# Performance work log

Measured on AMD Instinct MI355X. Metric: run time of the kernel, lower is better.

The kernel has to match this reference:

```python
import jax, jax.numpy as jnp
import numpy as np
import math

# ---- architecture constants (match init_kwargs defaults of OfficialMamba3SISO) ----
D_MODEL = 1024
D_STATE = 128
EXPAND = 2
HEADDIM = 64
NGROUPS = 1
D_INNER = EXPAND * D_MODEL              # 2048
NHEADS = D_INNER // HEADDIM             # 32
ROPE_FRACTION = 0.5
SPLIT = int(D_STATE * ROPE_FRACTION)    # rotary span of the state dim
SPLIT -= SPLIT % 2                      # 64
NUM_ANGLES = SPLIT // 2                 # 32
A_FLOOR = 1e-4
EPS = 1e-5
DT_MIN, DT_MAX, DT_INIT_FLOOR = 1e-3, 1e-1, 1e-4
D_IN_PROJ = 2 * D_INNER + 2 * D_STATE * NGROUPS + 3 * NHEADS + NUM_ANGLES  # 4480


def _rmsnorm(x, w):
    xf = x.astype(jnp.float32)
    return xf * jax.lax.rsqrt(jnp.mean(xf * xf, axis=-1, keepdims=True) + EPS) * w


def _rope(v, theta):
    # rotate first SPLIT dims of the state axis by cumulative angles theta [..., NUM_ANGLES]
    v1 = v[..., :NUM_ANGLES]
    v2 = v[..., NUM_ANGLES:SPLIT]
    rest = v[..., SPLIT:]
    c, s = jnp.cos(theta), jnp.sin(theta)
    return jnp.concatenate([v1 * c - v2 * s, v1 * s + v2 * c, rest], axis=-1)


def setup_inputs() -> dict:
    key = jax.random.key(0)
    ks = jax.random.split(key, 6)
    b, l = 2, 1024
    u = jax.random.normal(ks[0], (b, l, D_MODEL), jnp.float32)
    W_in = jax.random.normal(ks[1], (D_IN_PROJ, D_MODEL), jnp.float32) * 0.02
    W_out = jax.random.normal(ks[2], (D_MODEL, D_INNER), jnp.float32) * 0.02
    # dt_bias init exactly as in the torch module
    _dt = jnp.exp(jax.random.uniform(ks[3], (NHEADS,), jnp.float32)
                  * (math.log(DT_MAX) - math.log(DT_MIN)) + math.log(DT_MIN))
    _dt = jnp.clip(_dt, DT_INIT_FLOOR, None)
    dt_bias = _dt + jnp.log(-jnp.expm1(-_dt))
    B_bias = jnp.ones((NHEADS, D_STATE), jnp.float32)   # mimo_rank=1 squeezed
    C_bias = jnp.ones((NHEADS, D_STATE), jnp.float32)
    B_norm_w = jnp.ones((D_STATE,), jnp.float32)
    C_norm_w = jnp.ones((D_STATE,), jnp.float32)
    D_param = jnp.ones((NHEADS,), jnp.float32)
    return {"u": u, "W_in": W_in, "W_out": W_out, "dt_bias": dt_bias,
            "B_bias": B_bias, "C_bias": C_bias, "B_norm_w": B_norm_w,
            "C_norm_w": C_norm_w, "D_param": D_param}


def reference(u, W_in, W_out, dt_bias, B_bias, C_bias, B_norm_w, C_norm_w, D_param):
    b, l, _ = u.shape
    proj = u @ W_in.T                                   # [b,l,4480]
    sizes = [D_INNER, D_INNER, D_STATE * NGROUPS, D_STATE * NGROUPS,
             NHEADS, NHEADS, NHEADS, NUM_ANGLES]
    splits = np.cumsum(sizes)[:-1]
    z, x, B, C, dd_dt, dd_A, trap, angles = jnp.split(proj, splits, axis=-1)
    z = z.reshape(b, l, NHEADS, HEADDIM)
    x = x.reshape(b, l, NHEADS, HEADDIM)
    B = B.reshape(b, l, NGROUPS, D_STATE)
    C = C.reshape(b, l, NGROUPS, D_STATE)

    a = -jax.nn.softplus(dd_A.astype(jnp.float32))
    a = jnp.minimum(a, -A_FLOOR)                        # [b,l,h]
    dt = jax.nn.softplus(dd_dt.astype(jnp.float32) + dt_bias)  # [b,l,h]
    adt = a * dt

    # RoPE-style angle cumsum: theta_t = sum_{s<=t} angle_s * dt_s (per head)
    theta = jnp.cumsum(angles[:, :, None, :].astype(jnp.float32) * dt[..., None], axis=1)  # [b,l,h,na]

    Bn = _rmsnorm(B, B_norm_w)                          # [b,l,g,n]
    Cn = _rmsnorm(C, C_norm_w)
    head_group = np.repeat(np.arange(NGROUPS), NHEADS // NGROUPS)
    Bh = Bn[:, :, head_group, :] + B_bias               # [b,l,h,n]
    Ch = Cn[:, :, head_group, :] + C_bias
    Bh = _rope(Bh, theta)
    Ch = _rope(Ch, theta)

    lam = jax.nn.sigmoid(trap.astype(jnp.float32))      # trapezoidal mixing, [b,l,h]
    g = jnp.exp(adt)                                    # decay, [b,l,h]

    xs = (jnp.moveaxis(x.astype(jnp.float32), 1, 0), jnp.moveaxis(Bh, 1, 0),
          jnp.moveaxis(Ch, 1, 0), jnp.moveaxis(dt, 1, 0),
          jnp.moveaxis(g, 1, 0), jnp.moveaxis(lam, 1, 0))
    h0 = jnp.zeros((b, NHEADS, HEADDIM, D_STATE), jnp.float32)
    bx0 = jnp.zeros_like(h0)

    def step(carry, inp):
        h, bx_prev = carry
        x_t, B_t, C_t, dt_t, g_t, lam_t = inp
        bx_t = x_t[..., :, None] * B_t[..., None, :]    # outer product [b,h,p,n]
        ge = g_t[..., None, None]
        dte = dt_t[..., None, None]
        le = lam_t[..., None, None]
        # generalized trapezoidal discretization (Mamba-3):
        # h_t = g_t h_{t-1} + dt_t * (lam_t B_t x_t + (1-lam_t) g_t B_{t-1} x_{t-1})
        h = ge * h + dte * (le * bx_t + (1.0 - le) * ge * bx_prev)
        y_t = jnp.einsum('bhpn,bhn->bhp', h, C_t)
        return (h, bx_t), y_t

    _, ys = jax.lax.scan(step, (h0, bx0), xs)
    y = jnp.moveaxis(ys, 0, 1) + D_param[:, None] * x   # skip term, [b,l,h,p]
    y = y * jax.nn.silu(z)                              # gated output (Z passed to kernel)
    y = y.reshape(b, l, D_INNER).astype(u.dtype)
    return y @ W_out.T
```

## Files before the change

kernel.cpp:

```cpp
#include <hip/hip_runtime.h>
#include <hip/hip_bf16.h>
#include <math.h>

#define BATCH 2
#define SEQ 1024
#define DMODEL 1024
#define DSTATE 128
#define HEADDIM 64
#define NHEADS 32
#define DINNER 2048
#define NUMANG 32
#define DPROJ 4480
#define CH 64
#define NCH 16
#define TAILSTART 4352
#define OFF_Z 0
#define OFF_X 2048
#define OFF_B 4096
#define OFF_C 4224
#define OFF_DT 4352
#define OFF_A 4384
#define OFF_TRAP 4416
#define OFF_ANG 4448

typedef __attribute__((ext_vector_type(8))) short bf16x8;
typedef __attribute__((ext_vector_type(4))) float f32x4;
typedef unsigned short u16;

__device__ __forceinline__ u16 f2bf(float f) {
  unsigned int u = __float_as_uint(f);
  u += 0x7FFFu + ((u >> 16) & 1u);
  return (u16)(u >> 16);
}
__device__ __forceinline__ float bf2f(u16 x) {
  return __uint_as_float(((unsigned int)x) << 16);
}

#define N4_U 524288
#define N4_WI 1146880
#define N4_WO 524288

__global__ __launch_bounds__(256) void cvt_all(const float* __restrict__ u,
                                               const float* __restrict__ Wi,
                                               const float* __restrict__ Wo,
                                               u16* __restrict__ ub16,
                                               u16* __restrict__ Wi16,
                                               u16* __restrict__ Wo16) {
  int i = blockIdx.x * 256 + threadIdx.x;
  const float4* src;
  ushort4* dst;
  int idx;
  if (i < N4_U) { src = (const float4*)u; dst = (ushort4*)ub16; idx = i; }
  else if (i < N4_U + N4_WI) { src = (const float4*)Wi; dst = (ushort4*)Wi16; idx = i - N4_U; }
  else if (i < N4_U + N4_WI + N4_WO) { src = (const float4*)Wo; dst = (ushort4*)Wo16; idx = i - N4_U - N4_WI; }
  else return;
  float4 v = src[idx];
  ushort4 o;
  o.x = f2bf(v.x); o.y = f2bf(v.y); o.z = f2bf(v.z); o.w = f2bf(v.w);
  dst[idx] = o;
}

__device__ __forceinline__ void gload_lds16(const void* g, void* l) {
  __builtin_amdgcn_global_load_lds(
      (const __attribute__((address_space(1))) unsigned int*)g,
      (__attribute__((address_space(3))) unsigned int*)l, 16, 0, 0);
}

__global__ __launch_bounds__(256) void gemm_proj64(const u16* __restrict__ A,
                                                   const u16* __restrict__ B,
                                                   u16* __restrict__ Cb,
                                                   float* __restrict__ tailF,
                                                   int M, int N, int K) {
  __shared__ u16 As[64 * 64];
  __shared__ u16 Bs[64 * 64];
  const int tid = threadIdx.x;
  const int lane = tid & 63, wave = tid >> 6;
  const int bm = blockIdx.y * 64, bn = blockIdx.x * 64;
  const int wm = (wave >> 1) * 32, wn = (wave & 1) * 32;
  const int srow = wave * 8 + (lane >> 3);
  const int scol = (((lane & 7) ^ ((lane >> 3) & 7)) * 8);
  const u16* Ab = A + (size_t)(bm + srow) * K + scol;
  const u16* Bb = B + (size_t)(bn + srow) * K + scol;
  u16* Asw = As + wave * 512;
  u16* Bsw = Bs + wave * 512;
  f32x4 acc[2][2];
#pragma unroll
  for (int i = 0; i < 2; ++i)
#pragma unroll
    for (int j = 0; j < 2; ++j) acc[i][j] = (f32x4){0.f, 0.f, 0.f, 0.f};
  const int fr = lane & 15, fq = lane >> 4, sw = fr & 7;

  for (int k0 = 0; k0 < K; k0 += 64) {
    __syncthreads();
#pragma unroll
    for (int it = 0; it < 2; ++it) {
      gload_lds16(Ab + (size_t)(it * 32) * K + k0, Asw + it * 2048);
      gload_lds16(Bb + (size_t)(it * 32) * K + k0, Bsw + it * 2048);
    }
    __syncthreads();
#pragma unroll
    for (int kh = 0; kh < 2; ++kh) {
      bf16x8 af[2], bfv[2];
#pragma unroll
      for (int i = 0; i < 2; ++i)
        af[i] = *(const bf16x8*)(As + (wm + i * 16 + fr) * 64 + (((kh * 4 + fq) ^ sw) * 8));
#pragma unroll
      for (int j = 0; j < 2; ++j)
        bfv[j] = *(const bf16x8*)(Bs + (wn + j * 16 + fr) * 64 + (((kh * 4 + fq) ^ sw) * 8));
#pragma unroll
      for (int i = 0; i < 2; ++i)
#pragma unroll
        for (int j = 0; j < 2; ++j)
          acc[i][j] = __builtin_amdgcn_mfma_f32_16x16x32_bf16(af[i], bfv[j], acc[i][j], 0, 0, 0);
    }
  }
  const int orow = bm + wm + fq * 4;
  const int ocol = bn + wn + fr;
  const bool tail = (bn >= TAILSTART);
#pragma unroll
  for (int i = 0; i < 2; ++i)
#pragma unroll
    for (int j = 0; j < 2; ++j)
#pragma unroll
      for (int r = 0; r < 4; ++r) {
        float v = acc[i][j][r];
        int row = orow + i * 16 + r, col = ocol + j * 16;
        Cb[(size_t)row * N + col] = f2bf(v);
        if (tail) tailF[(size_t)row * 128 + (col - TAILSTART)] = v;
      }
}

__global__ __launch_bounds__(256) void gemm_out64(const u16* __restrict__ A,
                                                  const u16* __restrict__ B,
                                                  float* __restrict__ C,
                                                  int M, int N, int K) {
  __shared__ u16 As[64 * 64];
  __shared__ u16 Bs[64 * 64];
  const int tid = threadIdx.x;
  const int lane = tid & 63, wave = tid >> 6;
  const int bm = blockIdx.y * 64, bn = blockIdx.x * 64;
  const int wm = (wave >> 1) * 32, wn = (wave & 1) * 32;
  const int srow = wave * 8 + (lane >> 3);
  const int scol = (((lane & 7) ^ ((lane >> 3) & 7)) * 8);
  const u16* Ab = A + (size_t)(bm + srow) * K + scol;
  const u16* Bb = B + (size_t)(bn + srow) * K + scol;
  u16* Asw = As + wave * 512;
  u16* Bsw = Bs + wave * 512;
  f32x4 acc[2][2];
#pragma unroll
  for (int i = 0; i < 2; ++i)
#pragma unroll
    for (int j = 0; j < 2; ++j) acc[i][j] = (f32x4){0.f, 0.f, 0.f, 0.f};
  const int fr = lane & 15, fq = lane >> 4, sw = fr & 7;

  for (int k0 = 0; k0 < K; k0 += 64) {
    __syncthreads();
#pragma unroll
    for (int it = 0; it < 2; ++it) {
      gload_lds16(Ab + (size_t)(it * 32) * K + k0, Asw + it * 2048);
      gload_lds16(Bb + (size_t)(it * 32) * K + k0, Bsw + it * 2048);
    }
    __syncthreads();
#pragma unroll
    for (int kh = 0; kh < 2; ++kh) {
      bf16x8 af[2], bfv[2];
#pragma unroll
      for (int i = 0; i < 2; ++i)
        af[i] = *(const bf16x8*)(As + (wm + i * 16 + fr) * 64 + (((kh * 4 + fq) ^ sw) * 8));
#pragma unroll
      for (int j = 0; j < 2; ++j)
        bfv[j] = *(const bf16x8*)(Bs + (wn + j * 16 + fr) * 64 + (((kh * 4 + fq) ^ sw) * 8));
#pragma unroll
      for (int i = 0; i < 2; ++i)
#pragma unroll
        for (int j = 0; j < 2; ++j)
          acc[i][j] = __builtin_amdgcn_mfma_f32_16x16x32_bf16(af[i], bfv[j], acc[i][j], 0, 0, 0);
    }
  }
  const int orow = bm + wm + fq * 4;
  const int ocol = bn + wn + fr;
#pragma unroll
  for (int i = 0; i < 2; ++i)
#pragma unroll
    for (int j = 0; j < 2; ++j)
#pragma unroll
      for (int r = 0; r < 4; ++r)
        C[(size_t)(orow + i * 16 + r) * N + ocol + j * 16] = acc[i][j][r];
}

__device__ __forceinline__ float softplusf(float x) {
  return fmaxf(x, 0.f) + log1pf(expf(-fabsf(x)));
}

__global__ __launch_bounds__(1024) void theta_kernel(const float* __restrict__ tailF,
                                                     const float* __restrict__ dt_bias,
                                                     float4* __restrict__ sc4,
                                                     float4* __restrict__ theta4) {
  __shared__ float4 part[16];
  __shared__ float4 part2[16];
  const int blk = blockIdx.x;
  const int bh = blk >> 3, kc = blk & 7;
  const int b = bh >> 5, h = bh & 31;
  const int l = threadIdx.x;
  const int lane = l & 63, w = l >> 6;
  const float* trow = tailF + (size_t)(b * SEQ + l) * 128;
  float ddt = trow[h];
  float dt = softplusf(ddt + dt_bias[h]);
  if (kc == 0) {
    float dda = trow[32 + h];
    float trp = trow[64 + h];
    float a = fminf(-softplusf(dda), -1e-4f);
    float adt = a * dt;
    float lam = 1.0f / (1.0f + expf(-trp));
    sc4[(size_t)bh * SEQ + l] = make_float4(dt, expf(adt), lam, adt);
  }
  float4 v = *(const float4*)(trow + 96 + kc * 4);
  v.x *= dt; v.y *= dt; v.z *= dt; v.w *= dt;
#pragma unroll
  for (int off = 1; off < 64; off <<= 1) {
    float tx = __shfl_up(v.x, off, 64);
    float ty = __shfl_up(v.y, off, 64);
    float tz = __shfl_up(v.z, off, 64);
    float tw = __shfl_up(v.w, off, 64);
    if (lane >= off) { v.x += tx; v.y += ty; v.z += tz; v.w += tw; }
  }
  if (lane == 63) part[w] = v;
  __syncthreads();
  if (l < 16) {
    float4 p = part[l];
#pragma unroll
    for (int off = 1; off < 16; off <<= 1) {
      float tx = __shfl_up(p.x, off, 16);
      float ty = __shfl_up(p.y, off, 16);
      float tz = __shfl_up(p.z, off, 16);
      float tw = __shfl_up(p.w, off, 16);
      if (l >= off) { p.x += tx; p.y += ty; p.z += tz; p.w += tw; }
    }
    part2[l] = p;
  }
  __syncthreads();
  if (w > 0) {
    float4 o = part2[w - 1];
    v.x += o.x; v.y += o.y; v.z += o.z; v.w += o.w;
  }
  theta4[((size_t)(b * SEQ + l) * NHEADS + h) * 8 + kc] = v;
}

__global__ __launch_bounds__(1024) void rope_kernel(const u16* __restrict__ proj16,
                                                    const float* __restrict__ theta,
                                                    const float* __restrict__ B_bias,
                                                    const float* __restrict__ C_bias,
                                                    const float* __restrict__ Bnw,
                                                    const float* __restrict__ Cnw,
                                                    u16* __restrict__ Bh,
                                                    u16* __restrict__ Ch) {
  const int bl = blockIdx.x;
  const int b = bl >> 10, l = bl & 1023;
  const int tid = threadIdx.x;
  __shared__ float sB[128], sC[128], red[4];
  __shared__ float cth[1024], sth[1024];
  float bv = 0.f, cv = 0.f;
  const size_t row = (size_t)bl * DPROJ;
  if (tid < 128) {
    bv = bf2f(proj16[row + OFF_B + tid]);
    cv = bf2f(proj16[row + OFF_C + tid]);
    float sb = bv * bv, sc = cv * cv;
    for (int m = 32; m; m >>= 1) { sb += __shfl_xor(sb, m); sc += __shfl_xor(sc, m); }
    const int wave = tid >> 6;
    if ((tid & 63) == 0) { red[wave * 2] = sb; red[wave * 2 + 1] = sc; }
  }
  {
    float th = theta[(size_t)bl * 1024 + tid];
    cth[tid] = cosf(th);
    sth[tid] = sinf(th);
  }
  __syncthreads();
  if (tid < 128) {
    float rb = rsqrtf((red[0] + red[2]) / 128.0f + 1e-5f);
    float rc = rsqrtf((red[1] + red[3]) / 128.0f + 1e-5f);
    sB[tid] = bv * rb * Bnw[tid];
    sC[tid] = cv * rc * Cnw[tid];
  }
  __syncthreads();
  const int h = tid >> 5;
  const int n0 = (tid & 31) * 4;
  float ob[4], oc[4];
  if (n0 < 32) {
#pragma unroll
    for (int j = 0; j < 4; ++j) {
      int n = n0 + j;
      float c = cth[h * 32 + n], s = sth[h * 32 + n];
      float b1 = sB[n] + B_bias[h * 128 + n];
      float b2 = sB[n + 32] + B_bias[h * 128 + n + 32];
      float c1 = sC[n] + C_bias[h * 128 + n];
      float c2 = sC[n + 32] + C_bias[h * 128 + n + 32];
      ob[j] = b1 * c - b2 * s;
      oc[j] = c1 * c - c2 * s;
    }
  } else if (n0 < 64) {
#pragma unroll
    for (int j = 0; j < 4; ++j) {
      int n = n0 + j, k = n - 32;
      float c = cth[h * 32 + k], s = sth[h * 32 + k];
      float b1 = sB[k] + B_bias[h * 128 + k];
      float b2 = sB[k + 32] + B_bias[h * 128 + k + 32];
      float c1 = sC[k] + C_bias[h * 128 + k];
      float c2 = sC[k + 32] + C_bias[h * 128 + k + 32];
      ob[j] = b1 * s + b2 * c;
      oc[j] = c1 * s + c2 * c;
    }
  } else {
#pragma unroll
    for (int j = 0; j < 4; ++j) {
      int n = n0 + j;
      ob[j] = sB[n] + B_bias[h * 128 + n];
      oc[j] = sC[n] + C_bias[h * 128 + n];
    }
  }
  size_t o = (((size_t)(b * NHEADS + h)) * SEQ + l) * DSTATE + n0;
  ushort4 vb = {f2bf(ob[0]), f2bf(ob[1]), f2bf(ob[2]), f2bf(ob[3])};
  ushort4 vc = {f2bf(oc[0]), f2bf(oc[1]), f2bf(oc[2]), f2bf(oc[3])};
  *(ushort4*)&Bh[o] = vb;
  *(ushort4*)&Ch[o] = vc;
}

#define SWB 136
#define SWS 72

__global__ __launch_bounds__(256) void chunk_kernel(
    const u16* __restrict__ proj16,
    const float4* __restrict__ sc4,
    const u16* __restrict__ Bh16,
    const u16* __restrict__ Ch16,
    u16* __restrict__ Ybuf,
    u16* __restrict__ dHT16,
    float* __restrict__ Gv_g,
    float2* __restrict__ de_g) {
  __shared__ u16 sCb[64 * SWB];
  __shared__ u16 sBb[64 * SWB];
  __shared__ u16 sBt[128 * SWS];
  __shared__ u16 sXt[64 * SWS];
  __shared__ u16 sSw[64 * SWS];
  __shared__ float sA[64], sW[64], sDL[64], sCV[64];

  const int blk = blockIdx.x;
  const int bh = blk >> 4, ch = blk & 15;
  const int b = bh >> 5, h = bh & 31;
  const int t0 = ch * CH;
  const int tid = threadIdx.x;
  const int lane = tid & 63, wave = tid >> 6;

  {
    const int row = tid >> 5;
    const int c4 = tid & 31;
#pragma unroll
    for (int pass = 0; pass < 8; ++pass) {
      int ll = pass * 8 + row;
      int l = t0 + ll;
      ushort4 cv = *(const ushort4*)&Ch16[((size_t)bh * SEQ + l) * DSTATE + c4 * 4];
      ushort4 bv = *(const ushort4*)&Bh16[((size_t)bh * SEQ + l) * DSTATE + c4 * 4];
      *(ushort4*)&sCb[ll * SWB + c4 * 4] = cv;
      *(ushort4*)&sBb[ll * SWB + c4 * 4] = bv;
      sBt[(c4 * 4 + 0) * SWS + ll] = bv.x;
      sBt[(c4 * 4 + 1) * SWS + ll] = bv.y;
      sBt[(c4 * 4 + 2) * SWS + ll] = bv.z;
      sBt[(c4 * 4 + 3) * SWS + ll] = bv.w;
    }
    const int xr = tid >> 2, xc = tid & 3;
    const u16* xrow = &proj16[(size_t)(b * SEQ + t0 + xr) * DPROJ + OFF_X + h * 64];
#pragma unroll
    for (int j = 0; j < 4; ++j) {
      ushort4 xv = *(const ushort4*)(xrow + xc * 16 + j * 4);
      int p = xc * 16 + j * 4;
      sXt[(p + 0) * SWS + xr] = xv.x;
      sXt[(p + 1) * SWS + xr] = xv.y;
      sXt[(p + 2) * SWS + xr] = xv.z;
      sXt[(p + 3) * SWS + xr] = xv.w;
    }
  }
  if (tid < 64) {
    float4 s = sc4[(size_t)bh * SEQ + t0 + tid];
    float dt = s.x, lam = s.z, adt = s.w;
    float A = adt;
#pragma unroll
    for (int off = 1; off < 64; off <<= 1) {
      float t = __shfl_up(A, off, 64);
      if (tid >= off) A += t;
    }
    float dtn = __shfl_down(dt, 1, 64);
    float lamn = __shfl_down(lam, 1, 64);
    float dl = dt * lam;
    float w = dl + dtn * (1.0f - lamn);
    if (tid == 63) w = 0.0f;
    float A63 = __shfl(A, 63, 64);
    float cv = (tid < 63) ? expf(A63 - A) * w : dl;
    sA[tid] = A; sW[tid] = w; sCV[tid] = cv; sDL[tid] = dl;
    Gv_g[((size_t)bh * NCH + ch) * 64 + tid] = expf(A);
    if (tid == 0) de_g[(size_t)bh * NCH + ch] = make_float2(expf(A63), dt * (1.0f - lam));
  }
  __syncthreads();

  const int fr = lane & 15, fq = lane >> 4;

  {
    f32x4 acc[4];
#pragma unroll
    for (int j = 0; j < 4; ++j) acc[j] = (f32x4){0.f, 0.f, 0.f, 0.f};
#pragma unroll
    for (int kc = 0; kc < 4; ++kc) {
      bf16x8 af = *(const bf16x8*)&sBb[(wave * 16 + fr) * SWB + kc * 32 + fq * 8];
#pragma unroll
      for (int j = 0; j < 4; ++j) {
        bf16x8 bf = *(const bf16x8*)&sCb[(j * 16 + fr) * SWB + kc * 32 + fq * 8];
        acc[j] = __builtin_amdgcn_mfma_f32_16x16x32_bf16(af, bf, acc[j], 0, 0, 0);
      }
    }
    const int sbase = wave * 16 + fq * 4;
#pragma unroll
    for (int j = 0; j < 4; ++j) {
      int t = j * 16 + fr;
      float At = sA[t], dlt = sDL[t];
#pragma unroll
      for (int r = 0; r < 4; ++r) {
        int ss = sbase + r;
        float f = (ss < t) ? expf(At - sA[ss]) * sW[ss] : ((ss == t) ? dlt : 0.0f);
        sSw[t * SWS + ss] = f2bf(acc[j][r] * f);
      }
    }
  }
  __syncthreads();

  {
    f32x4 acc[4];
#pragma unroll
    for (int j = 0; j < 4; ++j) acc[j] = (f32x4){0.f, 0.f, 0.f, 0.f};
#pragma unroll
    for (int kc = 0; kc < 2; ++kc) {
      bf16x8 af = *(const bf16x8*)&sSw[(wave * 16 + fr) * SWS + kc * 32 + fq * 8];
#pragma unroll
      for (int j = 0; j < 4; ++j) {
        bf16x8 bf = *(const bf16x8*)&sXt[(j * 16 + fr) * SWS + kc * 32 + fq * 8];
        acc[j] = __builtin_amdgcn_mfma_f32_16x16x32_bf16(af, bf, acc[j], 0, 0, 0);
      }
    }
    const int tr = t0 + wave * 16 + fq * 4;
#pragma unroll
    for (int j = 0; j < 4; ++j) {
      int p = j * 16 + fr;
#pragma unroll
      for (int r = 0; r < 4; ++r)
        Ybuf[(size_t)(b * SEQ + tr + r) * DINNER + h * 64 + p] = f2bf(acc[j][r]);
    }
  }
  __syncthreads();

  {
    const int p = tid >> 2;
    const int s0 = (tid & 3) * 16;
#pragma unroll
    for (int k = 0; k < 16; ++k) {
      int s = s0 + k;
      sXt[p * SWS + s] = f2bf(bf2f(sXt[p * SWS + s]) * sCV[s]);
    }
  }
  __syncthreads();

  {
    f32x4 acc[8];
#pragma unroll
    for (int j = 0; j < 8; ++j) acc[j] = (f32x4){0.f, 0.f, 0.f, 0.f};
#pragma unroll
    for (int kc = 0; kc < 2; ++kc) {
      bf16x8 af = *(const bf16x8*)&sXt[(wave * 16 + fr) * SWS + kc * 32 + fq * 8];
#pragma unroll
      for (int j = 0; j < 8; ++j) {
        bf16x8 bf = *(const bf16x8*)&sBt[(j * 16 + fr) * SWS + kc * 32 + fq * 8];
        acc[j] = __builtin_amdgcn_mfma_f32_16x16x32_bf16(af, bf, acc[j], 0, 0, 0);
      }
    }
    const int pr = wave * 16 + fq * 4;
#pragma unroll
    for (int j = 0; j < 8; ++j) {
      int n = j * 16 + fr;
#pragma unroll
      for (int r = 0; r < 4; ++r)
        dHT16[(((size_t)bh * NCH + ch) * 64 + pr + r) * 128 + n] = f2bf(acc[j][r]);
    }
  }
}

__global__ __launch_bounds__(128) void carry_kernel(
    const u16* __restrict__ proj16,
    const u16* __restrict__ Bh16,
    const u16* __restrict__ dHT16,
    const float2* __restrict__ de_g,
    u16* __restrict__ Heff16) {
  const int blk = blockIdx.x;
  const int bh = blk >> 2, pg = blk & 3;
  const int b = bh >> 5, h = bh & 31;
  const int tid = threadIdx.x;
  const int p = pg * 16 + (tid >> 3);
  const int n0 = (tid & 7) * 16;
  float hreg[16] = {};
  for (int c = 0; c < NCH; ++c) {
    float2 de = de_g[bh * NCH + c];
    float heff[16];
    if (c == 0) {
#pragma unroll
      for (int j = 0; j < 16; ++j) heff[j] = 0.0f;
    } else {
      int lprev = c * CH - 1;
      float xp = bf2f(proj16[(size_t)(b * SEQ + lprev) * DPROJ + OFF_X + h * 64 + p]);
      float eBx = de.y * xp;
      const u16* Bp = &Bh16[((size_t)bh * SEQ + lprev) * DSTATE + n0];
#pragma unroll
      for (int j4 = 0; j4 < 4; ++j4) {
        ushort4 bv = *(const ushort4*)(Bp + j4 * 4);
        heff[j4 * 4 + 0] = hreg[j4 * 4 + 0] + eBx * bf2f(bv.x);
        heff[j4 * 4 + 1] = hreg[j4 * 4 + 1] + eBx * bf2f(bv.y);
        heff[j4 * 4 + 2] = hreg[j4 * 4 + 2] + eBx * bf2f(bv.z);
        heff[j4 * 4 + 3] = hreg[j4 * 4 + 3] + eBx * bf2f(bv.w);
      }
    }
    size_t base = (((size_t)bh * NCH + c) * 64 + p) * 128 + n0;
#pragma unroll
    for (int j4 = 0; j4 < 4; ++j4) {
      ushort4 o = {f2bf(heff[j4 * 4 + 0]), f2bf(heff[j4 * 4 + 1]),
                   f2bf(heff[j4 * 4 + 2]), f2bf(heff[j4 * 4 + 3])};
      *(ushort4*)&Heff16[base + j4 * 4] = o;
    }
#pragma unroll
    for (int j4 = 0; j4 < 4; ++j4) {
      ushort4 dh = *(const ushort4*)&dHT16[base + j4 * 4];
      hreg[j4 * 4 + 0] = de.x * heff[j4 * 4 + 0] + bf2f(dh.x);
      hreg[j4 * 4 + 1] = de.x * heff[j4 * 4 + 1] + bf2f(dh.y);
      hreg[j4 * 4 + 2] = de.x * heff[j4 * 4 + 2] + bf2f(dh.z);
      hreg[j4 * 4 + 3] = de.x * heff[j4 * 4 + 3] + bf2f(dh.w);
    }
  }
}

__global__ __launch_bounds__(256) void inter_kernel(
    const u16* __restrict__ proj16,
    const u16* __restrict__ Ch16,
    const u16* __restrict__ Heff16,
    const float* __restrict__ Gv_g,
    const float* __restrict__ Dp,
    u16* __restrict__ Ybuf) {
  __shared__ u16 sCt[64 * SWB];
  __shared__ u16 sHe[64 * SWB];
  __shared__ float sGv[64];
  const int blk = blockIdx.x;
  const int bh = blk >> 4, ch = blk & 15;
  const int b = bh >> 5, h = bh & 31;
  const int t0 = ch * CH;
  const int tid = threadIdx.x;
  const int lane = tid & 63, wave = tid >> 6;
  {
    const int row = tid >> 2, seg = tid & 3;
    const u16* csrc = &Ch16[((size_t)bh * SEQ + t0 + row) * DSTATE + seg * 32];
    const u16* hsrc = &Heff16[(((size_t)bh * NCH + ch) * 64 + row) * 128 + seg * 32];
#pragma unroll
    for (int q = 0; q < 4; ++q) {
      *(ushort4*)&sCt[row * SWB + seg * 32 + q * 8]     = *(const ushort4*)(csrc + q * 8);
      *(ushort4*)&sCt[row * SWB + seg * 32 + q * 8 + 4] = *(const ushort4*)(csrc + q * 8 + 4);
      *(ushort4*)&sHe[row * SWB + seg * 32 + q * 8]     = *(const ushort4*)(hsrc + q * 8);
      *(ushort4*)&sHe[row * SWB + seg * 32 + q * 8 + 4] = *(const ushort4*)(hsrc + q * 8 + 4);
    }
    if (tid < 64) sGv[tid] = Gv_g[((size_t)bh * NCH + ch) * 64 + tid];
  }
  __syncthreads();
  const int fr = lane & 15, fq = lane >> 4;
  f32x4 acc[4];
#pragma unroll
  for (int j = 0; j < 4; ++j) acc[j] = (f32x4){0.f, 0.f, 0.f, 0.f};
#pragma unroll
  for (int kc = 0; kc < 4; ++kc) {
    bf16x8 af = *(const bf16x8*)&sCt[(wave * 16 + fr) * SWB + kc * 32 + fq * 8];
#pragma unroll
    for (int j = 0; j < 4; ++j) {
      bf16x8 bf = *(const bf16x8*)&sHe[(j * 16 + fr) * SWB + kc * 32 + fq * 8];
      acc[j] = __builtin_amdgcn_mfma_f32_16x16x32_bf16(af, bf, acc[j], 0, 0, 0);
    }
  }
  const float Dv = Dp[h];
#pragma unroll
  for (int r = 0; r < 4; ++r) {
    int tl = wave * 16 + fq * 4 + r;
    int l = t0 + tl;
    float gt = sGv[tl];
    size_t rowp = (size_t)(b * SEQ + l) * DPROJ;
    size_t yrow = (size_t)(b * SEQ + l) * DINNER + h * 64;
#pragma unroll
    for (int j = 0; j < 4; ++j) {
      int p = j * 16 + fr;
      float x = bf2f(proj16[rowp + OFF_X + h * 64 + p]);
      float z = bf2f(proj16[rowp + OFF_Z + h * 64 + p]);
      float y1 = bf2f(Ybuf[yrow + p]);
      float yy = y1 + gt * acc[j][r] + Dv * x;
      float sg = 1.0f / (1.0f + expf(-z));
      Ybuf[yrow + p] = f2bf(yy * z * sg);
    }
  }
}

extern "C" void kernel_launch(void* const* d_in, const int* in_sizes, int n_in,
                              void* d_out, int out_size, void* d_ws, size_t ws_size,
                              hipStream_t stream) {
  const float* u       = (const float*)d_in[0];
  const float* W_in    = (const float*)d_in[1];
  const float* W_out   = (const float*)d_in[2];
  const float* dt_bias = (const float*)d_in[3];
  const float* B_bias  = (const float*)d_in[4];
  const float* C_bias  = (const float*)d_in[5];
  const float* Bnw     = (const float*)d_in[6];
  const float* Cnw     = (const float*)d_in[7];
  const float* Dp      = (const float*)d_in[8];
  float* out = (float*)d_out;

  char* ws = (char*)d_ws;
  u16*    proj16 = (u16*)(ws);
  float*  tailF  = (float*)(ws + 18350080);
  float4* sc4    = (float4*)(ws + 19398656);
  float*  theta  = (float*)(ws + 20447232);
  u16*    Bh16   = (u16*)(ws + 28835840);
  u16*    Ch16   = (u16*)(ws + 45613056);
  u16*    Ybuf   = (u16*)(ws + 62390272);
  u16*    dHT16  = (u16*)(ws + 70778880);
  u16*    Heff16 = (u16*)(ws + 87556096);
  float*  Gv     = (float*)(ws + 104333312);
  float2* deg    = (float2*)(ws + 104595456);
  u16*    ub16   = (u16*)(ws + 104603648);
  u16*    Wi16   = (u16*)(ws + 108797952);
  u16*    Wo16   = (u16*)(ws + 117972992);

  cvt_all<<<(N4_U + N4_WI + N4_WO + 255) / 256, 256, 0, stream>>>(
      u, W_in, W_out, ub16, Wi16, Wo16);
  gemm_proj64<<<dim3(DPROJ / 64, (BATCH * SEQ) / 64), 256, 0, stream>>>(
      ub16, Wi16, proj16, tailF, BATCH * SEQ, DPROJ, DMODEL);
  theta_kernel<<<BATCH * NHEADS * 8, 1024, 0, stream>>>(tailF, dt_bias, sc4, (float4*)theta);
  rope_kernel<<<BATCH * SEQ, 1024, 0, stream>>>(proj16, theta, B_bias, C_bias, Bnw, Cnw, Bh16, Ch16);
  chunk_kernel<<<BATCH * NHEADS * NCH, 256, 0, stream>>>(
      proj16, sc4, Bh16, Ch16, Ybuf, dHT16, Gv, deg);
  carry_kernel<<<BATCH * NHEADS * 4, 128, 0, stream>>>(proj16, Bh16, dHT16, deg, Heff16);
  inter_kernel<<<BATCH * NHEADS * NCH, 256, 0, stream>>>(
      proj16, Ch16, Heff16, Gv, Dp, Ybuf);
  gemm_out64<<<dim3(DMODEL / 64, (BATCH * SEQ) / 64), 256, 0, stream>>>(
      Ybuf, Wo16, out, BATCH * SEQ, DMODEL, DINNER);
}
```

Before: 231.0 us.

## Fuse RMSNorm and RoPE of B/C into chunk kernel, drop rope kernel

Removes the separate rope kernel and computes RMSNorm, bias and rotary embedding of B and C per chunk inside chunk_kernel, reading raw projections directly. The full per-head B tensor is no longer written; only the last row of each chunk is saved for carry_kernel, while C is still written for inter_kernel. This saves a launch and a large global write/read round trip. In exchange chunk_kernel does redundant cos/sin and normalisation work per head and adds two extra barriers, and the theta layout changes to per (b,h) rows.

```diff
diff --git a/kernel.cpp b/kernel.cpp
--- a/kernel.cpp
+++ b/kernel.cpp
@@ -243,85 +243,7 @@
     float4 o = part2[w - 1];
     v.x += o.x; v.y += o.y; v.z += o.z; v.w += o.w;
   }
-  theta4[((size_t)(b * SEQ + l) * NHEADS + h) * 8 + kc] = v;
-}
-
-__global__ __launch_bounds__(1024) void rope_kernel(const u16* __restrict__ proj16,
-                                                    const float* __restrict__ theta,
-                                                    const float* __restrict__ B_bias,
-                                                    const float* __restrict__ C_bias,
-                                                    const float* __restrict__ Bnw,
-                                                    const float* __restrict__ Cnw,
-                                                    u16* __restrict__ Bh,
-                                                    u16* __restrict__ Ch) {
-  const int bl = blockIdx.x;
-  const int b = bl >> 10, l = bl & 1023;
-  const int tid = threadIdx.x;
-  __shared__ float sB[128], sC[128], red[4];
-  __shared__ float cth[1024], sth[1024];
-  float bv = 0.f, cv = 0.f;
-  const size_t row = (size_t)bl * DPROJ;
-  if (tid < 128) {
-    bv = bf2f(proj16[row + OFF_B + tid]);
-    cv = bf2f(proj16[row + OFF_C + tid]);
-    float sb = bv * bv, sc = cv * cv;
-    for (int m = 32; m; m >>= 1) { sb += __shfl_xor(sb, m); sc += __shfl_xor(sc, m); }
-    const int wave = tid >> 6;
-    if ((tid & 63) == 0) { red[wave * 2] = sb; red[wave * 2 + 1] = sc; }
-  }
-  {
-    float th = theta[(size_t)bl * 1024 + tid];
-    cth[tid] = cosf(th);
-    sth[tid] = sinf(th);
-  }
-  __syncthreads();
-  if (tid < 128) {
-    float rb = rsqrtf((red[0] + red[2]) / 128.0f + 1e-5f);
-    float rc = rsqrtf((red[1] + red[3]) / 128.0f + 1e-5f);
-    sB[tid] = bv * rb * Bnw[tid];
-    sC[tid] = cv * rc * Cnw[tid];
-  }
-  __syncthreads();
-  const int h = tid >> 5;
-  const int n0 = (tid & 31) * 4;
-  float ob[4], oc[4];
-  if (n0 < 32) {
-#pragma unroll
-    for (int j = 0; j < 4; ++j) {
-      int n = n0 + j;
-      float c = cth[h * 32 + n], s = sth[h * 32 + n];
-      float b1 = sB[n] + B_bias[h * 128 + n];
-      float b2 = sB[n + 32] + B_bias[h * 128 + n + 32];
-      float c1 = sC[n] + C_bias[h * 128 + n];
-      float c2 = sC[n + 32] + C_bias[h * 128 + n + 32];
-      ob[j] = b1 * c - b2 * s;
-      oc[j] = c1 * c - c2 * s;
-    }
-  } else if (n0 < 64) {
-#pragma unroll
-    for (int j = 0; j < 4; ++j) {
-      int n = n0 + j, k = n - 32;
-      float c = cth[h * 32 + k], s = sth[h * 32 + k];
-      float b1 = sB[k] + B_bias[h * 128 + k];
-      float b2 = sB[k + 32] + B_bias[h * 128 + k + 32];
-      float c1 = sC[k] + C_bias[h * 128 + k];
-      float c2 = sC[k + 32] + C_bias[h * 128 + k + 32];
-      ob[j] = b1 * s + b2 * c;
-      oc[j] = c1 * s + c2 * c;
-    }
-  } else {
-#pragma unroll
-    for (int j = 0; j < 4; ++j) {
-      int n = n0 + j;
-      ob[j] = sB[n] + B_bias[h * 128 + n];
-      oc[j] = sC[n] + C_bias[h * 128 + n];
-    }
-  }
-  size_t o = (((size_t)(b * NHEADS + h)) * SEQ + l) * DSTATE + n0;
-  ushort4 vb = {f2bf(ob[0]), f2bf(ob[1]), f2bf(ob[2]), f2bf(ob[3])};
-  ushort4 vc = {f2bf(oc[0]), f2bf(oc[1]), f2bf(oc[2]), f2bf(oc[3])};
-  *(ushort4*)&Bh[o] = vb;
-  *(ushort4*)&Ch[o] = vc;
+  theta4[((size_t)bh * SEQ + l) * 8 + kc] = v;
 }
 
 #define SWB 136
@@ -330,8 +252,13 @@
 __global__ __launch_bounds__(256) void chunk_kernel(
     const u16* __restrict__ proj16,
     const float4* __restrict__ sc4,
-    const u16* __restrict__ Bh16,
-    const u16* __restrict__ Ch16,
+    const float* __restrict__ theta,
+    const float* __restrict__ B_bias,
+    const float* __restrict__ C_bias,
+    const float* __restrict__ Bnw,
+    const float* __restrict__ Cnw,
+    u16* __restrict__ Ch16,
+    u16* __restrict__ Bbound,
     u16* __restrict__ Ybuf,
     u16* __restrict__ dHT16,
     float* __restrict__ Gv_g,
@@ -342,6 +269,7 @@
   __shared__ u16 sXt[64 * SWS];
   __shared__ u16 sSw[64 * SWS];
   __shared__ float sA[64], sW[64], sDL[64], sCV[64];
+  __shared__ float sRb[64], sRc[64];
 
   const int blk = blockIdx.x;
   const int bh = blk >> 4, ch = blk & 15;
@@ -351,31 +279,35 @@
   const int lane = tid & 63, wave = tid >> 6;
 
   {
-    const int row = tid >> 5;
-    const int c4 = tid & 31;
-#pragma unroll
-    for (int pass = 0; pass < 8; ++pass) {
-      int ll = pass * 8 + row;
-      int l = t0 + ll;
-      ushort4 cv = *(const ushort4*)&Ch16[((size_t)bh * SEQ + l) * DSTATE + c4 * 4];
-      ushort4 bv = *(const ushort4*)&Bh16[((size_t)bh * SEQ + l) * DSTATE + c4 * 4];
-      *(ushort4*)&sCb[ll * SWB + c4 * 4] = cv;
-      *(ushort4*)&sBb[ll * SWB + c4 * 4] = bv;
-      sBt[(c4 * 4 + 0) * SWS + ll] = bv.x;
-      sBt[(c4 * 4 + 1) * SWS + ll] = bv.y;
-      sBt[(c4 * 4 + 2) * SWS + ll] = bv.z;
-      sBt[(c4 * 4 + 3) * SWS + ll] = bv.w;
-    }
-    const int xr = tid >> 2, xc = tid & 3;
-    const u16* xrow = &proj16[(size_t)(b * SEQ + t0 + xr) * DPROJ + OFF_X + h * 64];
+    const int r = tid >> 2, seg = tid & 3, n0s = seg * 32;
+    const size_t prow = (size_t)(b * SEQ + t0 + r) * DPROJ;
+    float ssB = 0.f, ssC = 0.f;
+#pragma unroll
+    for (int q = 0; q < 8; ++q) {
+      ushort4 bu = *(const ushort4*)&proj16[prow + OFF_B + n0s + q * 4];
+      ushort4 cu = *(const ushort4*)&proj16[prow + OFF_C + n0s + q * 4];
+      *(ushort4*)&sBb[r * SWB + n0s + q * 4] = bu;
+      *(ushort4*)&sCb[r * SWB + n0s + q * 4] = cu;
+      float b0 = bf2f(bu.x), b1 = bf2f(bu.y), b2 = bf2f(bu.z), b3 = bf2f(bu.w);
+      float c0 = bf2f(cu.x), c1 = bf2f(cu.y), c2 = bf2f(cu.z), c3 = bf2f(cu.w);
+      ssB += b0 * b0 + b1 * b1 + b2 * b2 + b3 * b3;
+      ssC += c0 * c0 + c1 * c1 + c2 * c2 + c3 * c3;
+    }
+    ssB += __shfl_xor(ssB, 1); ssB += __shfl_xor(ssB, 2);
+    ssC += __shfl_xor(ssC, 1); ssC += __shfl_xor(ssC, 2);
+    if (seg == 0) {
+      sRb[r] = rsqrtf(ssB / 128.f + 1e-5f);
+      sRc[r] = rsqrtf(ssC / 128.f + 1e-5f);
+    }
+    const u16* xrow = &proj16[prow + OFF_X + h * 64];
 #pragma unroll
     for (int j = 0; j < 4; ++j) {
-      ushort4 xv = *(const ushort4*)(xrow + xc * 16 + j * 4);
-      int p = xc * 16 + j * 4;
-      sXt[(p + 0) * SWS + xr] = xv.x;
-      sXt[(p + 1) * SWS + xr] = xv.y;
-      sXt[(p + 2) * SWS + xr] = xv.z;
-      sXt[(p + 3) * SWS + xr] = xv.w;
+      ushort4 xv = *(const ushort4*)(xrow + seg * 16 + j * 4);
+      int p = seg * 16 + j * 4;
+      sXt[(p + 0) * SWS + r] = xv.x;
+      sXt[(p + 1) * SWS + r] = xv.y;
+      sXt[(p + 2) * SWS + r] = xv.z;
+      sXt[(p + 3) * SWS + r] = xv.w;
     }
   }
   if (tid < 64) {
@@ -400,6 +332,69 @@
   }
   __syncthreads();
 
+  ushort4 bout[8], cout[8];
+  {
+    const int r2 = tid & 63, seg2 = tid >> 6, n0b = seg2 * 32;
+    const float rb = sRb[r2], rc = sRc[r2];
+    const float* thr = &theta[(size_t)(bh * SEQ + t0 + r2) * 32];
+#pragma unroll
+    for (int q8 = 0; q8 < 8; ++q8) {
+      u16 tb[4], tc[4];
+#pragma unroll
+      for (int jj = 0; jj < 4; ++jj) {
+        int n = n0b + q8 * 4 + jj;
+        float oB, oC;
+        if (n < 64) {
+          int k = n & 31;
+          float th = thr[k];
+          float cc = cosf(th), ssn = sinf(th);
+          float b1 = bf2f(sBb[r2 * SWB + k]) * rb * Bnw[k] + B_bias[h * 128 + k];
+          float b2 = bf2f(sBb[r2 * SWB + k + 32]) * rb * Bnw[k + 32] + B_bias[h * 128 + k + 32];
+          float c1 = bf2f(sCb[r2 * SWB + k]) * rc * Cnw[k] + C_bias[h * 128 + k];
+          float c2 = bf2f(sCb[r2 * SWB + k + 32]) * rc * Cnw[k + 32] + C_bias[h * 128 + k + 32];
+          if (n < 32) { oB = b1 * cc - b2 * ssn; oC = c1 * cc - c2 * ssn; }
+          else        { oB = b1 * ssn + b2 * cc; oC = c1 * ssn + c2 * cc; }
+        } else {
+          oB = bf2f(sBb[r2 * SWB + n]) * rb * Bnw[n] + B_bias[h * 128 + n];
+          oC = bf2f(sCb[r2 * SWB + n]) * rc * Cnw[n] + C_bias[h * 128 + n];
+        }
+        tb[jj] = f2bf(oB);
+        tc[jj] = f2bf(oC);
+      }
+      bout[q8] = make_ushort4(tb[0], tb[1], tb[2], tb[3]);
+      cout[q8] = make_ushort4(tc[0], tc[1], tc[2], tc[3]);
+    }
+  }
+  __syncthreads();
+
+  {
+    const int r2 = tid & 63, seg2 = tid >> 6, n0b = seg2 * 32;
+#pragma unroll
+    for (int q8 = 0; q8 < 8; ++q8) {
+      *(ushort4*)&sBb[r2 * SWB + n0b + q8 * 4] = bout[q8];
+      *(ushort4*)&sCb[r2 * SWB + n0b + q8 * 4] = cout[q8];
+      int nb = n0b + q8 * 4;
+      sBt[(nb + 0) * SWS + r2] = bout[q8].x;
+      sBt[(nb + 1) * SWS + r2] = bout[q8].y;
+      sBt[(nb + 2) * SWS + r2] = bout[q8].z;
+      sBt[(nb + 3) * SWS + r2] = bout[q8].w;
+    }
+    if (r2 == 63) {
+#pragma unroll
+      for (int q8 = 0; q8 < 8; ++q8)
+        *(ushort4*)&Bbound[((size_t)bh * NCH + ch) * 128 + n0b + q8 * 4] = bout[q8];
+    }
+  }
+  __syncthreads();
+
+  {
+    const int r = tid >> 2, seg = tid & 3, n0s = seg * 32;
+#pragma unroll
+    for (int q = 0; q < 8; ++q)
+      *(ushort4*)&Ch16[((size_t)bh * SEQ + t0 + r) * DSTATE + n0s + q * 4] =
+          *(const ushort4*)&sCb[r * SWB + n0s + q * 4];
+  }
+
   const int fr = lane & 15, fq = lane >> 4;
 
   {
@@ -491,7 +486,7 @@
 
 __global__ __launch_bounds__(128) void carry_kernel(
     const u16* __restrict__ proj16,
-    const u16* __restrict__ Bh16,
+    const u16* __restrict__ Bbound,
     const u16* __restrict__ dHT16,
     const float2* __restrict__ de_g,
     u16* __restrict__ Heff16) {
@@ -512,7 +507,7 @@
       int lprev = c * CH - 1;
       float xp = bf2f(proj16[(size_t)(b * SEQ + lprev) * DPROJ + OFF_X + h * 64 + p]);
       float eBx = de.y * xp;
-      const u16* Bp = &Bh16[((size_t)bh * SEQ + lprev) * DSTATE + n0];
+      const u16* Bp = &Bbound[((size_t)bh * NCH + (c - 1)) * 128 + n0];
 #pragma unroll
       for (int j4 = 0; j4 < 4; ++j4) {
         ushort4 bv = *(const ushort4*)(Bp + j4 * 4);
@@ -623,26 +618,25 @@
   float*  tailF  = (float*)(ws + 18350080);
   float4* sc4    = (float4*)(ws + 19398656);
   float*  theta  = (float*)(ws + 20447232);
-  u16*    Bh16   = (u16*)(ws + 28835840);
-  u16*    Ch16   = (u16*)(ws + 45613056);
-  u16*    Ybuf   = (u16*)(ws + 62390272);
-  u16*    dHT16  = (u16*)(ws + 70778880);
-  u16*    Heff16 = (u16*)(ws + 87556096);
-  float*  Gv     = (float*)(ws + 104333312);
-  float2* deg    = (float2*)(ws + 104595456);
-  u16*    ub16   = (u16*)(ws + 104603648);
-  u16*    Wi16   = (u16*)(ws + 108797952);
-  u16*    Wo16   = (u16*)(ws + 117972992);
+  u16*    Ch16   = (u16*)(ws + 28835840);
+  u16*    Ybuf   = (u16*)(ws + 45613056);
+  u16*    dHT16  = (u16*)(ws + 54001664);
+  u16*    Heff16 = (u16*)(ws + 70778880);
+  float*  Gv     = (float*)(ws + 87556096);
+  float2* deg    = (float2*)(ws + 87818240);
+  u16*    Bbound = (u16*)(ws + 87826432);
+  u16*    ub16   = (u16*)(ws + 88088576);
+  u16*    Wi16   = (u16*)(ws + 92282880);
+  u16*    Wo16   = (u16*)(ws + 101457920);
 
   cvt_all<<<(N4_U + N4_WI + N4_WO + 255) / 256, 256, 0, stream>>>(
       u, W_in, W_out, ub16, Wi16, Wo16);
   gemm_proj64<<<dim3(DPROJ / 64, (BATCH * SEQ) / 64), 256, 0, stream>>>(
       ub16, Wi16, proj16, tailF, BATCH * SEQ, DPROJ, DMODEL);
   theta_kernel<<<BATCH * NHEADS * 8, 1024, 0, stream>>>(tailF, dt_bias, sc4, (float4*)theta);
-  rope_kernel<<<BATCH * SEQ, 1024, 0, stream>>>(proj16, theta, B_bias, C_bias, Bnw, Cnw, Bh16, Ch16);
   chunk_kernel<<<BATCH * NHEADS * NCH, 256, 0, stream>>>(
-      proj16, sc4, Bh16, Ch16, Ybuf, dHT16, Gv, deg);
-  carry_kernel<<<BATCH * NHEADS * 4, 128, 0, stream>>>(proj16, Bh16, dHT16, deg, Heff16);
+      proj16, sc4, theta, B_bias, C_bias, Bnw, Cnw, Ch16, Bbound, Ybuf, dHT16, Gv, deg);
+  carry_kernel<<<BATCH * NHEADS * 4, 128, 0, stream>>>(proj16, Bbound, dHT16, deg, Heff16);
   inter_kernel<<<BATCH * NHEADS * NCH, 256, 0, stream>>>(
       proj16, Ch16, Heff16, Gv, Dp, Ybuf);
   gemm_out64<<<dim3(DMODEL / 64, (BATCH * SEQ) / 64), 256, 0, stream>>>(
```

New measurement: 253.2 us. +9.6%, slower.

## Double-buffer LDS tiles in projection GEMMs to overlap loads with MFMA

Applied to the files above, without the earlier changes.

Both bf16 GEMM kernels now keep two LDS buffers for the A and B tiles. The first tile is prefetched before the loop, and the next K-slice is issued with global_load_lds into the other buffer before the MFMA work on the current one. This drops one barrier per iteration and is meant to hide global-load latency behind compute. In exchange, LDS use per block doubles, which could lower occupancy, and an unused offset variable is left in the code.

```diff
diff --git a/kernel.cpp b/kernel.cpp
--- a/kernel.cpp
+++ b/kernel.cpp
@@ -71,8 +71,8 @@
                                                    u16* __restrict__ Cb,
                                                    float* __restrict__ tailF,
                                                    int M, int N, int K) {
-  __shared__ u16 As[64 * 64];
-  __shared__ u16 Bs[64 * 64];
+  __shared__ u16 As[2][64 * 64];
+  __shared__ u16 Bs[2][64 * 64];
   const int tid = threadIdx.x;
   const int lane = tid & 63, wave = tid >> 6;
   const int bm = blockIdx.y * 64, bn = blockIdx.x * 64;
@@ -81,8 +81,8 @@
   const int scol = (((lane & 7) ^ ((lane >> 3) & 7)) * 8);
   const u16* Ab = A + (size_t)(bm + srow) * K + scol;
   const u16* Bb = B + (size_t)(bn + srow) * K + scol;
-  u16* Asw = As + wave * 512;
-  u16* Bsw = Bs + wave * 512;
+  const int soff = wave * 512 + (lane & 7) * 8 + (lane >> 3) * 64;
+  (void)soff;
   f32x4 acc[2][2];
 #pragma unroll
   for (int i = 0; i < 2; ++i)
@@ -90,23 +90,34 @@
     for (int j = 0; j < 2; ++j) acc[i][j] = (f32x4){0.f, 0.f, 0.f, 0.f};
   const int fr = lane & 15, fq = lane >> 4, sw = fr & 7;
 
-  for (int k0 = 0; k0 < K; k0 += 64) {
+#pragma unroll
+  for (int it = 0; it < 2; ++it) {
+    gload_lds16(Ab + (size_t)(it * 32) * K, &As[0][wave * 512 + it * 2048]);
+    gload_lds16(Bb + (size_t)(it * 32) * K, &Bs[0][wave * 512 + it * 2048]);
+  }
+
+  const int NIT = K >> 6;
+  for (int itk = 0; itk < NIT; ++itk) {
+    const int cur = itk & 1;
     __syncthreads();
-#pragma unroll
-    for (int it = 0; it < 2; ++it) {
-      gload_lds16(Ab + (size_t)(it * 32) * K + k0, Asw + it * 2048);
-      gload_lds16(Bb + (size_t)(it * 32) * K + k0, Bsw + it * 2048);
-    }
-    __syncthreads();
+    if (itk + 1 < NIT) {
+      const int nk = (itk + 1) << 6;
+      const int nxt = cur ^ 1;
+#pragma unroll
+      for (int it = 0; it < 2; ++it) {
+        gload_lds16(Ab + (size_t)(it * 32) * K + nk, &As[nxt][wave * 512 + it * 2048]);
+        gload_lds16(Bb + (size_t)(it * 32) * K + nk, &Bs[nxt][wave * 512 + it * 2048]);
+      }
+    }
 #pragma unroll
     for (int kh = 0; kh < 2; ++kh) {
       bf16x8 af[2], bfv[2];
 #pragma unroll
       for (int i = 0; i < 2; ++i)
-        af[i] = *(const bf16x8*)(As + (wm + i * 16 + fr) * 64 + (((kh * 4 + fq) ^ sw) * 8));
+        af[i] = *(const bf16x8*)(&As[cur][(wm + i * 16 + fr) * 64 + (((kh * 4 + fq) ^ sw) * 8)]);
 #pragma unroll
       for (int j = 0; j < 2; ++j)
-        bfv[j] = *(const bf16x8*)(Bs + (wn + j * 16 + fr) * 64 + (((kh * 4 + fq) ^ sw) * 8));
+        bfv[j] = *(const bf16x8*)(&Bs[cur][(wn + j * 16 + fr) * 64 + (((kh * 4 + fq) ^ sw) * 8)]);
 #pragma unroll
       for (int i = 0; i < 2; ++i)
 #pragma unroll
@@ -134,8 +145,8 @@
                                                   const u16* __restrict__ B,
                                                   float* __restrict__ C,
                                                   int M, int N, int K) {
-  __shared__ u16 As[64 * 64];
-  __shared__ u16 Bs[64 * 64];
+  __shared__ u16 As[2][64 * 64];
+  __shared__ u16 Bs[2][64 * 64];
   const int tid = threadIdx.x;
   const int lane = tid & 63, wave = tid >> 6;
   const int bm = blockIdx.y * 64, bn = blockIdx.x * 64;
@@ -144,8 +155,6 @@
   const int scol = (((lane & 7) ^ ((lane >> 3) & 7)) * 8);
   const u16* Ab = A + (size_t)(bm + srow) * K + scol;
   const u16* Bb = B + (size_t)(bn + srow) * K + scol;
-  u16* Asw = As + wave * 512;
-  u16* Bsw = Bs + wave * 512;
   f32x4 acc[2][2];
 #pragma unroll
   for (int i = 0; i < 2; ++i)
@@ -153,23 +162,33 @@
     for (int j = 0; j < 2; ++j) acc[i][j] = (f32x4){0.f, 0.f, 0.f, 0.f};
   const int fr = lane & 15, fq = lane >> 4, sw = fr & 7;
 
-  for (int k0 = 0; k0 < K; k0 += 64) {
+#pragma unroll
+  for (int it = 0; it < 2; ++it) {
+    gload_lds16(Ab + (size_t)(it * 32) * K, &As[0][wave * 512 + it * 2048]);
+    gload_lds16(Bb + (size_t)(it * 32) * K, &Bs[0][wave * 512 + it * 2048]);
+  }
+  const int NIT = K >> 6;
+  for (int itk = 0; itk < NIT; ++itk) {
+    const int cur = itk & 1;
     __syncthreads();
-#pragma unroll
-    for (int it = 0; it < 2; ++it) {
-      gload_lds16(Ab + (size_t)(it * 32) * K + k0, Asw + it * 2048);
-      gload_lds16(Bb + (size_t)(it * 32) * K + k0, Bsw + it * 2048);
-    }
-    __syncthreads();
+    if (itk + 1 < NIT) {
+      const int nk = (itk + 1) << 6;
+      const int nxt = cur ^ 1;
+#pragma unroll
+      for (int it = 0; it < 2; ++it) {
+        gload_lds16(Ab + (size_t)(it * 32) * K + nk, &As[nxt][wave * 512 + it * 2048]);
+        gload_lds16(Bb + (size_t)(it * 32) * K + nk, &Bs[nxt][wave * 512 + it * 2048]);
+      }
+    }
 #pragma unroll
     for (int kh = 0; kh < 2; ++kh) {
       bf16x8 af[2], bfv[2];
 #pragma unroll
       for (int i = 0; i < 2; ++i)
-        af[i] = *(const bf16x8*)(As + (wm + i * 16 + fr) * 64 + (((kh * 4 + fq) ^ sw) * 8));
+        af[i] = *(const bf16x8*)(&As[cur][(wm + i * 16 + fr) * 64 + (((kh * 4 + fq) ^ sw) * 8)]);
 #pragma unroll
       for (int j = 0; j < 2; ++j)
-        bfv[j] = *(const bf16x8*)(Bs + (wn + j * 16 + fr) * 64 + (((kh * 4 + fq) ^ sw) * 8));
+        bfv[j] = *(const bf16x8*)(&Bs[cur][(wn + j * 16 + fr) * 64 + (((kh * 4 + fq) ^ sw) * 8)]);
 #pragma unroll
       for (int i = 0; i < 2; ++i)
 #pragma unroll
```

After: 231.8 us. Within noise of the previous version (+0.3%).
